# Kernel optimization log

Measured on AMD Instinct MI355X. Metric: run time of the kernel, lower is better.

Reference implementation:

```python
import jax, jax.numpy as jnp
import numpy as np

B, L, D, H = 4, 2048, 1024, 16
DH = D // H


def setup_inputs() -> dict:
    key = jax.random.key(0)
    ks = jax.random.split(key, 16)
    s = 1.0 / np.sqrt(D)
    return {
        "query": jax.random.normal(ks[0], (B, L, D), jnp.float32),
        "key_": jax.random.normal(ks[1], (B, L, D), jnp.float32),
        "value": jax.random.normal(ks[2], (B, L, D), jnp.float32),
        "mask": jax.random.randint(ks[3], (B, L), 0, 2, jnp.int32),
        "Wq": jax.random.normal(ks[4], (D, D), jnp.float32) * s,
        "bq": jnp.zeros((D,), jnp.float32),
        "Wk": jax.random.normal(ks[5], (D, D), jnp.float32) * s,
        "bk": jnp.zeros((D,), jnp.float32),
        "Wv": jax.random.normal(ks[6], (D, D), jnp.float32) * s,
        "bv": jnp.zeros((D,), jnp.float32),
        "Wo": jax.random.normal(ks[7], (D, D), jnp.float32) * s,
        "bo": jnp.zeros((D,), jnp.float32),
        "gamma": jnp.ones((D,), jnp.float32),
        "beta": jnp.zeros((D,), jnp.float32),
    }


def reference(query, key_, value, mask, Wq, bq, Wk, bk, Wv, bv, Wo, bo, gamma, beta):
    old_query = query
    # projections (Linear: x @ W^T + b)
    q = query @ Wq.T + bq            # [B,L,D]
    k = key_ @ Wk.T + bk
    v = value @ Wv.T + bv
    # split heads -> [B,H,L,DH]
    q = q.reshape(B, L, H, DH).transpose(0, 2, 1, 3)
    k = k.reshape(B, L, H, DH).transpose(0, 2, 1, 3)
    v = v.reshape(B, L, H, DH).transpose(0, 2, 1, 3)
    scores = jnp.einsum("bhqd,bhkd->bhqk", q, k) / jnp.sqrt(jnp.float32(DH))
    m = mask[:, None, None, :]        # [B,1,1,L]
    scores = jnp.where(m == 0, jnp.float32(-1e9), scores)
    attn = jax.nn.softmax(scores, axis=-1)
    out = jnp.einsum("bhqk,bhkd->bhqd", attn, v)
    out = out.transpose(0, 2, 1, 3).reshape(B, L, D)
    out = out @ Wo.T + bo
    # dropout is identity in eval; residual + layernorm (eps=1e-5)
    x = out + old_query
    mu = jnp.mean(x, axis=-1, keepdims=True)
    var = jnp.var(x, axis=-1, keepdims=True)
    return (x - mu) / jnp.sqrt(var + 1e-5) * gamma + beta
```

## Files before the change

### kernel.cpp

```cpp
#include <hip/hip_runtime.h>
#include <hip/hip_bf16.h>

typedef __attribute__((ext_vector_type(4))) float f32x4;
typedef __attribute__((ext_vector_type(16))) float f32x16;
typedef __attribute__((ext_vector_type(2))) unsigned int u32x2;
typedef __attribute__((ext_vector_type(4))) unsigned int u32x4;
typedef __attribute__((ext_vector_type(8))) __bf16 bf16x8;

__device__ inline unsigned short f2bf(float x) {
    return __builtin_bit_cast(unsigned short, (__bf16)x);
}
__device__ inline unsigned int pack2(float lo, float hi) {
    return (unsigned int)f2bf(lo) | ((unsigned int)f2bf(hi) << 16);
}
__device__ inline u32x4 cvt8(const float* __restrict__ p) {
    f32x4 a = *(const f32x4*)p;
    f32x4 b = *(const f32x4*)(p + 4);
    u32x4 r;
    r[0] = pack2(a[0], a[1]);
    r[1] = pack2(a[2], a[3]);
    r[2] = pack2(b[0], b[1]);
    r[3] = pack2(b[2], b[3]);
    return r;
}
__device__ inline bf16x8 ldfrag(const unsigned short* p) {
    u32x4 t = *(const u32x4*)p;
    return __builtin_bit_cast(bf16x8, t);
}

__global__ __launch_bounds__(256) void cvt_w3(
    const float* __restrict__ wq, const float* __restrict__ wk,
    const float* __restrict__ wv, unsigned short* __restrict__ dst)
{
    const float* s = blockIdx.y == 0 ? wq : (blockIdx.y == 1 ? wk : wv);
    unsigned short* d = dst + (size_t)blockIdx.y * 1048576;
    const int i = blockIdx.x * 256 + threadIdx.x;
    const int n = i >> 7;
    const int kg = (i >> 2) & 31;
    const int slot = (i & 3) ^ ((n >> 1) & 3);
    *(u32x4*)(d + (((size_t)n << 10) | (kg << 5) | (slot << 3))) =
        cvt8(s + (size_t)i * 8);
}
__global__ __launch_bounds__(256) void cvt_w1(
    const float* __restrict__ src, unsigned short* __restrict__ dst)
{
    const int i = blockIdx.x * 256 + threadIdx.x;
    const int n = i >> 7;
    const int kg = (i >> 2) & 31;
    const int slot = (i & 3) ^ ((n >> 1) & 3);
    *(u32x4*)(dst + (((size_t)n << 10) | (kg << 5) | (slot << 3))) =
        cvt8(src + (size_t)i * 8);
}

__global__ __launch_bounds__(256) void gemm_qkv(
    const float* __restrict__ Aq, const float* __restrict__ Ak,
    const float* __restrict__ Av, const unsigned short* __restrict__ W16,
    const float* __restrict__ bq, const float* __restrict__ bk,
    const float* __restrict__ bv, unsigned short* __restrict__ Qb,
    unsigned short* __restrict__ Kb, unsigned short* __restrict__ Vtb,
    float qscale)
{
    __shared__ unsigned short Al[2][128][40];
    __shared__ unsigned short Bl[2][128][32];
    const int z = blockIdx.z;
    const float* Ap = z == 0 ? Aq : (z == 1 ? Ak : Av);
    const unsigned short* Bw = W16 + (size_t)z * 1048576;
    const float* bias = z == 0 ? bq : (z == 1 ? bk : bv);
    const float alpha = z == 0 ? qscale : 1.0f;

    const int tid = threadIdx.x;
    const int lane = tid & 63, w = tid >> 6;
    const int wr = w >> 1, wc = w & 1;
    const int m0 = blockIdx.x * 128, n0 = blockIdx.y * 128;
    const int fr = lane & 15, fq = lane >> 4;
    const int fqs = (fq ^ ((fr >> 1) & 3)) * 8;

    f32x4 acc[4][4] = {};
    f32x4 apreA[2][2], apreB[2][2];

    auto issueB = [&](int p, int k0) {
#pragma unroll
        for (int j = 0; j < 2; ++j) {
            const int f = (w * 2 + j) * 512 + lane * 8;
            const int r = f >> 5, c = f & 31;
            __builtin_amdgcn_global_load_lds(
                (const __attribute__((address_space(1))) void*)(Bw + (size_t)(n0 + r) * 1024 + k0 + c),
                (__attribute__((address_space(3))) void*)(&Bl[p][0][0] + (w * 2 + j) * 512),
                16, 0, 0);
        }
    };
    auto loadA = [&](f32x4 (&ap)[2][2], int k0) {
#pragma unroll
        for (int i = 0; i < 2; ++i) {
            const int e = (i * 256 + tid) * 8;
            const int r = e >> 5, c = e & 31;
            const float* src = Ap + (size_t)(m0 + r) * 1024 + k0 + c;
            ap[i][0] = *(const f32x4*)src;
            ap[i][1] = *(const f32x4*)(src + 4);
        }
    };
    auto stepBody = [&](int k0, f32x4 (&ap)[2][2], int p) {
#pragma unroll
        for (int i = 0; i < 2; ++i) {
            const int e = (i * 256 + tid) * 8;
            const int r = e >> 5, c = e & 31;
            u32x4 v;
            v[0] = pack2(ap[i][0][0], ap[i][0][1]);
            v[1] = pack2(ap[i][0][2], ap[i][0][3]);
            v[2] = pack2(ap[i][1][0], ap[i][1][1]);
            v[3] = pack2(ap[i][1][2], ap[i][1][3]);
            *(u32x4*)&Al[p][r][c] = v;
        }
        __syncthreads();
        if (k0 + 32 < 1024) issueB(p ^ 1, k0 + 32);
        if (k0 + 64 < 1024) loadA(ap, k0 + 64);

        bf16x8 af[4], bfv[4];
#pragma unroll
        for (int mt = 0; mt < 4; ++mt)
            af[mt] = ldfrag(&Al[p][wr * 64 + mt * 16 + fr][8 * fq]);
#pragma unroll
        for (int nt = 0; nt < 4; ++nt)
            bfv[nt] = ldfrag(&Bl[p][wc * 64 + nt * 16 + fr][fqs]);
#pragma unroll
        for (int mt = 0; mt < 4; ++mt)
#pragma unroll
            for (int nt = 0; nt < 4; ++nt)
                acc[mt][nt] = __builtin_amdgcn_mfma_f32_16x16x32_bf16(af[mt], bfv[nt], acc[mt][nt], 0, 0, 0);
    };

    loadA(apreA, 0);
    loadA(apreB, 32);
    issueB(0, 0);

    for (int k0 = 0; k0 < 1024; k0 += 64) {
        stepBody(k0, apreA, 0);
        stepBody(k0 + 32, apreB, 1);
    }

#pragma unroll
    for (int mt = 0; mt < 4; ++mt) {
#pragma unroll
        for (int nt = 0; nt < 4; ++nt) {
            const int col = n0 + wc * 64 + nt * 16 + fr;
            const float bb = bias[col];
            const int row0 = m0 + wr * 64 + mt * 16 + fq * 4;
            if (z == 2) {
                float v0 = acc[mt][nt][0] + bb, v1 = acc[mt][nt][1] + bb;
                float v2 = acc[mt][nt][2] + bb, v3 = acc[mt][nt][3] + bb;
                const int bb_ = row0 >> 11, key = row0 & 2047;
                const int key2 = (key & ~12) | ((key & 4) << 1) | ((key & 8) >> 1);
                const int dh = col & 63;
                const int gg = ((dh ^ (dh >> 3)) & 7) << 3;
                const size_t idx = ((size_t)bb_ * 1024 + col) * 2048 + (key2 ^ gg);
                u32x2 pv;
                pv[0] = pack2(v0, v1);
                pv[1] = pack2(v2, v3);
                *(u32x2*)(Vtb + idx) = pv;
            } else if (z == 1) {
#pragma unroll
                for (int r = 0; r < 4; ++r) {
                    const int row = row0 + r;
                    const int tm = row & 127;
                    const int gg = ((tm ^ (tm >> 3)) & 7) << 3;
                    const size_t idx = (size_t)row * 1024 + ((col & ~63) | ((col & 63) ^ gg));
                    Kb[idx] = f2bf(acc[mt][nt][r] + bb);
                }
            } else {
#pragma unroll
                for (int r = 0; r < 4; ++r) {
                    const size_t idx = (size_t)(row0 + r) * 1024 + col;
                    Qb[idx] = f2bf((acc[mt][nt][r] + bb) * alpha);
                }
            }
        }
    }
}

__global__ __launch_bounds__(256) void gemm_out(
    const unsigned short* __restrict__ A, const unsigned short* __restrict__ Bw,
    const float* __restrict__ bias, const float* __restrict__ resid,
    float* __restrict__ Cp)
{
    __shared__ unsigned short Al[2][128][32];
    __shared__ unsigned short Bl[2][128][32];
    const int tid = threadIdx.x;
    const int lane = tid & 63, w = tid >> 6;
    const int wr = w >> 1, wc = w & 1;
    const int m0 = blockIdx.x * 128, n0 = blockIdx.y * 128;
    const int fr = lane & 15, fq = lane >> 4;
    const int fqs = (fq ^ ((fr >> 1) & 3)) * 8;

    f32x4 acc[4][4] = {};

    auto stage = [&](int p, int k0) {
#pragma unroll
        for (int j = 0; j < 2; ++j) {
            const int f = (w * 2 + j) * 512 + lane * 8;
            const int r = f >> 5, c = f & 31;
            __builtin_amdgcn_global_load_lds(
                (const __attribute__((address_space(1))) void*)(A + (size_t)(m0 + r) * 1024 + k0 + c),
                (__attribute__((address_space(3))) void*)(&Al[p][0][0] + (w * 2 + j) * 512),
                16, 0, 0);
            __builtin_amdgcn_global_load_lds(
                (const __attribute__((address_space(1))) void*)(Bw + (size_t)(n0 + r) * 1024 + k0 + c),
                (__attribute__((address_space(3))) void*)(&Bl[p][0][0] + (w * 2 + j) * 512),
                16, 0, 0);
        }
    };

    stage(0, 0);

    for (int k0 = 0; k0 < 1024; k0 += 32) {
        const int p = (k0 >> 5) & 1;
        __syncthreads();
        if (k0 + 32 < 1024) stage(p ^ 1, k0 + 32);

        bf16x8 af[4], bfv[4];
#pragma unroll
        for (int mt = 0; mt < 4; ++mt)
            af[mt] = ldfrag(&Al[p][wr * 64 + mt * 16 + fr][fqs]);
#pragma unroll
        for (int nt = 0; nt < 4; ++nt)
            bfv[nt] = ldfrag(&Bl[p][wc * 64 + nt * 16 + fr][fqs]);
#pragma unroll
        for (int mt = 0; mt < 4; ++mt)
#pragma unroll
            for (int nt = 0; nt < 4; ++nt)
                acc[mt][nt] = __builtin_amdgcn_mfma_f32_16x16x32_bf16(af[mt], bfv[nt], acc[mt][nt], 0, 0, 0);
    }

#pragma unroll
    for (int mt = 0; mt < 4; ++mt) {
#pragma unroll
        for (int nt = 0; nt < 4; ++nt) {
            const int col = n0 + wc * 64 + nt * 16 + fr;
            const float bb = bias[col];
            const int row0 = m0 + wr * 64 + mt * 16 + fq * 4;
#pragma unroll
            for (int r = 0; r < 4; ++r) {
                const size_t idx = (size_t)(row0 + r) * 1024 + col;
                Cp[idx] = acc[mt][nt][r] + bb + resid[idx];
            }
        }
    }
}

__global__ __launch_bounds__(256, 2) void attn_fwd(
    const unsigned short* __restrict__ K, const unsigned short* __restrict__ Q,
    const unsigned short* __restrict__ Vt_g, const int* __restrict__ mask,
    unsigned short* __restrict__ O)
{
    __shared__ unsigned short Kl[2][128][64];
    __shared__ unsigned short Vl[2][64][128];
    __shared__ unsigned short mlb[2][128];
    const int tid = threadIdx.x, lane = tid & 63, w = tid >> 6;
    const int l31 = lane & 31, hi = lane >> 5;
    const int qb = blockIdx.y >> 3;
    const int bh = ((blockIdx.y & 7) << 3) | blockIdx.x;
    const int q0 = qb * 256;
    const int b = bh >> 4;
    const size_t rowbase = (size_t)b * 2048;
    const int hoff = (bh & 15) * 64;
    const size_t vbase = (size_t)bh * 64 * 2048;

    const u32x4 onesu = {0x3F803F80u, 0x3F803F80u, 0x3F803F80u, 0x3F803F80u};
    const bf16x8 vones = __builtin_bit_cast(bf16x8, onesu);

    bf16x8 aq[2][4];
#pragma unroll
    for (int a = 0; a < 2; ++a) {
        const unsigned short* qp = Q + (rowbase + q0 + w * 64 + a * 32 + l31) * 1024 + hoff + hi * 8;
#pragma unroll
        for (int kk = 0; kk < 4; ++kk) aq[a][kk] = ldfrag(qp + kk * 16);
    }
    f32x16 o[2][2] = {};
    f32x16 os[2] = {};

    auto stageKV = [&](int p, int kb2) {
#pragma unroll
        for (int j = 0; j < 4; ++j) {
            const int q = w * 4 + j;
            const int hK = q * 512 + lane * 8;
            const int rK = hK >> 6, cK = hK & 63;
            __builtin_amdgcn_global_load_lds(
                (const __attribute__((address_space(1))) void*)(K + (rowbase + kb2 + rK) * 1024 + hoff + cK),
                (__attribute__((address_space(3))) void*)(&Kl[p][0][0] + q * 512),
                16, 0, 0);
            const int rV = hK >> 7, cV = hK & 127;
            __builtin_amdgcn_global_load_lds(
                (const __attribute__((address_space(1))) void*)(Vt_g + vbase + (size_t)rV * 2048 + kb2 + cV),
                (__attribute__((address_space(3))) void*)(&Vl[p][0][0] + q * 512),
                16, 0, 0);
        }
    };

    stageKV(0, 0);
    int mpre = (tid < 128) ? mask[rowbase + tid] : 0;
    if (tid < 128) mlb[0][tid] = f2bf(mpre == 0 ? -30000.0f : 0.0f);
    __syncthreads();

    for (int kb = 0, it = 0; kb < 2048; kb += 128, ++it) {
        const int p = it & 1;
        if (kb + 128 < 2048) {
            stageKV(p ^ 1, kb + 128);
            if (tid < 128) mpre = mask[rowbase + kb + 128 + tid];
        }

#pragma unroll
        for (int t = 0; t < 4; ++t) {
            const int swt = ((l31 ^ ((l31 >> 3) + t * 4)) & 7) << 3;
            const unsigned int mv = (hi == 0) ? (unsigned int)mlb[p][t * 32 + l31] : 0u;
            const u32x4 mfu = {mv, 0u, 0u, 0u};
            const bf16x8 kfm = __builtin_bit_cast(bf16x8, mfu);

            f32x16 z0 = {}, z1 = {};
            __builtin_amdgcn_s_setprio(1);
            z0 = __builtin_amdgcn_mfma_f32_32x32x16_bf16(kfm, vones, z0, 0, 0, 0);
            z1 = __builtin_amdgcn_mfma_f32_32x32x16_bf16(kfm, vones, z1, 0, 0, 0);
#pragma unroll
            for (int kk = 0; kk < 4; ++kk) {
                bf16x8 kf = ldfrag(&Kl[p][t * 32 + l31][(kk * 16 + hi * 8) ^ swt]);
                z0 = __builtin_amdgcn_mfma_f32_32x32x16_bf16(kf, aq[0][kk], z0, 0, 0, 0);
                z1 = __builtin_amdgcn_mfma_f32_32x32x16_bf16(kf, aq[1][kk], z1, 0, 0, 0);
            }
            __builtin_amdgcn_s_setprio(0);

            unsigned int pk[2][4][2];
#pragma unroll
            for (int g = 0; g < 4; ++g) {
                {
                    float p0 = __builtin_amdgcn_exp2f(z0[g * 4 + 0]);
                    float p1 = __builtin_amdgcn_exp2f(z0[g * 4 + 1]);
                    float p2 = __builtin_amdgcn_exp2f(z0[g * 4 + 2]);
                    float p3 = __builtin_amdgcn_exp2f(z0[g * 4 + 3]);
                    pk[0][g][0] = pack2(p0, p1);
                    pk[0][g][1] = pack2(p2, p3);
                }
                {
                    float p0 = __builtin_amdgcn_exp2f(z1[g * 4 + 0]);
                    float p1 = __builtin_amdgcn_exp2f(z1[g * 4 + 1]);
                    float p2 = __builtin_amdgcn_exp2f(z1[g * 4 + 2]);
                    float p3 = __builtin_amdgcn_exp2f(z1[g * 4 + 3]);
                    pk[1][g][0] = pack2(p0, p1);
                    pk[1][g][1] = pack2(p2, p3);
                }
            }

#pragma unroll
            for (int half = 0; half < 2; ++half) {
                const int c = t * 2 + half, G = half * 2;
                u32x4 fu0 = {pk[0][G][0], pk[0][G][1], pk[0][G + 1][0], pk[0][G + 1][1]};
                u32x4 fu1 = {pk[1][G][0], pk[1][G][1], pk[1][G + 1][0], pk[1][G + 1][1]};
                bf16x8 pf0 = __builtin_bit_cast(bf16x8, fu0);
                bf16x8 pf1 = __builtin_bit_cast(bf16x8, fu1);
                __builtin_amdgcn_s_setprio(1);
#pragma unroll
                for (int dt = 0; dt < 2; ++dt) {
                    const int swd = ((l31 ^ ((l31 >> 3) + dt * 4)) & 7) << 3;
                    bf16x8 vb = ldfrag(&Vl[p][dt * 32 + l31][(c * 16 + hi * 8) ^ swd]);
                    o[0][dt] = __builtin_amdgcn_mfma_f32_32x32x16_bf16(pf0, vb, o[0][dt], 0, 0, 0);
                    o[1][dt] = __builtin_amdgcn_mfma_f32_32x32x16_bf16(pf1, vb, o[1][dt], 0, 0, 0);
                }
                os[0] = __builtin_amdgcn_mfma_f32_32x32x16_bf16(pf0, vones, os[0], 0, 0, 0);
                os[1] = __builtin_amdgcn_mfma_f32_32x32x16_bf16(pf1, vones, os[1], 0, 0, 0);
                __builtin_amdgcn_s_setprio(0);
            }
        }

        if (kb + 128 < 2048 && tid < 128)
            mlb[p ^ 1][tid] = f2bf(mpre == 0 ? -30000.0f : 0.0f);
        __syncthreads();
    }

#pragma unroll
    for (int a = 0; a < 2; ++a)
#pragma unroll
        for (int g = 0; g < 4; ++g)
#pragma unroll
            for (int j = 0; j < 4; ++j) {
                const float inv = 1.0f / os[a][g * 4 + j];
                const size_t row = rowbase + q0 + w * 64 + a * 32 + g * 8 + hi * 4 + j;
                const int key = (int)((row >> 1) & 3);
                const int l31s = (l31 & 7) | ((((l31 >> 3) ^ key) & 3) << 3);
#pragma unroll
                for (int dt = 0; dt < 2; ++dt)
                    O[row * 1024 + hoff + dt * 32 + l31s] = f2bf(o[a][dt][g * 4 + j] * inv);
            }
}

__global__ __launch_bounds__(256) void ln_inplace(
    float* __restrict__ X, const float* __restrict__ gamma, const float* __restrict__ beta)
{
    __shared__ float red[8];
    const int tid = threadIdx.x, lane = tid & 63, w = tid >> 6;
    float* p = X + (size_t)blockIdx.x * 1024;
    f32x4 v = *((const f32x4*)p + tid);
    float s = v[0] + v[1] + v[2] + v[3];
    float s2 = v[0] * v[0] + v[1] * v[1] + v[2] * v[2] + v[3] * v[3];
#pragma unroll
    for (int d = 1; d < 64; d <<= 1) {
        s += __shfl_xor(s, d);
        s2 += __shfl_xor(s2, d);
    }
    if (lane == 0) { red[w] = s; red[4 + w] = s2; }
    __syncthreads();
    s = red[0] + red[1] + red[2] + red[3];
    s2 = red[4] + red[5] + red[6] + red[7];
    const float mu = s * (1.0f / 1024.0f);
    const float var = s2 * (1.0f / 1024.0f) - mu * mu;
    const float rstd = rsqrtf(var + 1e-5f);
    f32x4 g = *((const f32x4*)gamma + tid);
    f32x4 be = *((const f32x4*)beta + tid);
    f32x4 out;
#pragma unroll
    for (int j = 0; j < 4; ++j) out[j] = (v[j] - mu) * rstd * g[j] + be[j];
    *((f32x4*)p + tid) = out;
}

extern "C" void kernel_launch(void* const* d_in, const int* in_sizes, int n_in,
                              void* d_out, int out_size, void* d_ws, size_t ws_size,
                              hipStream_t stream) {
    const float* query = (const float*)d_in[0];
    const float* key_  = (const float*)d_in[1];
    const float* value = (const float*)d_in[2];
    const int*   mask  = (const int*)d_in[3];
    const float* Wq = (const float*)d_in[4];
    const float* bq = (const float*)d_in[5];
    const float* Wk = (const float*)d_in[6];
    const float* bk = (const float*)d_in[7];
    const float* Wv = (const float*)d_in[8];
    const float* bv = (const float*)d_in[9];
    const float* Wo = (const float*)d_in[10];
    const float* bo = (const float*)d_in[11];
    const float* gamma = (const float*)d_in[12];
    const float* beta  = (const float*)d_in[13];

    const size_t MD = (size_t)8192 * 1024;
    unsigned short* Qb  = (unsigned short*)d_ws;
    unsigned short* Kb  = Qb + MD;
    unsigned short* Vtb = Kb + MD;
    unsigned short* Ab  = Vtb + MD;
    float* out = (float*)d_out;
    unsigned short* W16 = (unsigned short*)d_out;
    unsigned short* Wo16 = Vtb;

    const float qscale = 0.125f * 1.4426950408889634f;

    cvt_w3<<<dim3(512, 3), 256, 0, stream>>>(Wq, Wk, Wv, W16);
    gemm_qkv<<<dim3(64, 8, 3), 256, 0, stream>>>(
        query, key_, value, W16, bq, bk, bv, Qb, Kb, Vtb, qscale);

    attn_fwd<<<dim3(8, 64), 256, 0, stream>>>(Kb, Qb, Vtb, mask, Ab);

    cvt_w1<<<512, 256, 0, stream>>>(Wo, Wo16);
    gemm_out<<<dim3(64, 8), 256, 0, stream>>>(Ab, Wo16, bo, query, out);
    ln_inplace<<<8192, 256, 0, stream>>>(out, gamma, beta);
}
```

Baseline: 230.5 us.

## Load QKV GEMM A operand straight from global into MFMA fragments, dropping LDS staging

The fp32 activation tile in the QKV projection GEMM is no longer converted and staged through shared memory. Each wave now loads its own A fragments directly from global memory, converts them to bf16 in registers, and prefetches one k-step ahead. This removes the LDS writes and reads for A and halves LDS usage. In exchange, A rows are loaded redundantly by the two column-waves, giving twice the global/L2 traffic for A, and the register footprint grows.

```diff
diff --git a/kernel.cpp b/kernel.cpp
--- a/kernel.cpp
+++ b/kernel.cpp
@@ -60,7 +60,6 @@
     unsigned short* __restrict__ Kb, unsigned short* __restrict__ Vtb,
     float qscale)
 {
-    __shared__ unsigned short Al[2][128][40];
     __shared__ unsigned short Bl[2][128][32];
     const int z = blockIdx.z;
     const float* Ap = z == 0 ? Aq : (z == 1 ? Ak : Av);
@@ -76,7 +75,7 @@
     const int fqs = (fq ^ ((fr >> 1) & 3)) * 8;
 
     f32x4 acc[4][4] = {};
-    f32x4 apreA[2][2], apreB[2][2];
+    f32x4 sX[4][2], sY[4][2];
 
     auto issueB = [&](int p, int k0) {
 #pragma unroll
@@ -89,36 +88,30 @@
                 16, 0, 0);
         }
     };
-    auto loadA = [&](f32x4 (&ap)[2][2], int k0) {
-#pragma unroll
-        for (int i = 0; i < 2; ++i) {
-            const int e = (i * 256 + tid) * 8;
-            const int r = e >> 5, c = e & 31;
-            const float* src = Ap + (size_t)(m0 + r) * 1024 + k0 + c;
-            ap[i][0] = *(const f32x4*)src;
-            ap[i][1] = *(const f32x4*)(src + 4);
+    auto loadAF = [&](f32x4 (&s)[4][2], int k0) {
+#pragma unroll
+        for (int mt = 0; mt < 4; ++mt) {
+            const float* p = Ap + (size_t)(m0 + wr * 64 + mt * 16 + fr) * 1024 + k0 + 8 * fq;
+            s[mt][0] = *(const f32x4*)p;
+            s[mt][1] = *(const f32x4*)(p + 4);
         }
     };
-    auto stepBody = [&](int k0, f32x4 (&ap)[2][2], int p) {
-#pragma unroll
-        for (int i = 0; i < 2; ++i) {
-            const int e = (i * 256 + tid) * 8;
-            const int r = e >> 5, c = e & 31;
+    auto stepBody = [&](int k0, f32x4 (&cur)[4][2], f32x4 (&nxt)[4][2], int p) {
+        __syncthreads();
+        if (k0 + 32 < 1024) {
+            issueB(p ^ 1, k0 + 32);
+            loadAF(nxt, k0 + 32);
+        }
+        bf16x8 af[4], bfv[4];
+#pragma unroll
+        for (int mt = 0; mt < 4; ++mt) {
             u32x4 v;
-            v[0] = pack2(ap[i][0][0], ap[i][0][1]);
-            v[1] = pack2(ap[i][0][2], ap[i][0][3]);
-            v[2] = pack2(ap[i][1][0], ap[i][1][1]);
-            v[3] = pack2(ap[i][1][2], ap[i][1][3]);
-            *(u32x4*)&Al[p][r][c] = v;
-        }
-        __syncthreads();
-        if (k0 + 32 < 1024) issueB(p ^ 1, k0 + 32);
-        if (k0 + 64 < 1024) loadA(ap, k0 + 64);
-
-        bf16x8 af[4], bfv[4];
-#pragma unroll
-        for (int mt = 0; mt < 4; ++mt)
-            af[mt] = ldfrag(&Al[p][wr * 64 + mt * 16 + fr][8 * fq]);
+            v[0] = pack2(cur[mt][0][0], cur[mt][0][1]);
+            v[1] = pack2(cur[mt][0][2], cur[mt][0][3]);
+            v[2] = pack2(cur[mt][1][0], cur[mt][1][1]);
+            v[3] = pack2(cur[mt][1][2], cur[mt][1][3]);
+            af[mt] = __builtin_bit_cast(bf16x8, v);
+        }
 #pragma unroll
         for (int nt = 0; nt < 4; ++nt)
             bfv[nt] = ldfrag(&Bl[p][wc * 64 + nt * 16 + fr][fqs]);
@@ -129,13 +122,12 @@
                 acc[mt][nt] = __builtin_amdgcn_mfma_f32_16x16x32_bf16(af[mt], bfv[nt], acc[mt][nt], 0, 0, 0);
     };
 
-    loadA(apreA, 0);
-    loadA(apreB, 32);
     issueB(0, 0);
+    loadAF(sX, 0);
 
     for (int k0 = 0; k0 < 1024; k0 += 64) {
-        stepBody(k0, apreA, 0);
-        stepBody(k0 + 32, apreB, 1);
+        stepBody(k0, sX, sY, 0);
+        stepBody(k0 + 32, sY, sX, 1);
     }
 
 #pragma unroll
```

Measured after the change: 354.1 us. 53.6% more time.
